# Kernel tuning notes

Measured on AMD Instinct MI355X. Metric: run time of the kernel, lower is better.

## Reference

```python
import jax, jax.numpy as jnp
import numpy as np


def setup_inputs() -> dict:
    key = jax.random.key(0)
    k1, k2 = jax.random.split(key)
    B, N, M, D = 16, 2048, 2048, 128
    Q = jax.random.normal(k1, (B, N, D), dtype=jnp.float32)
    KV = jax.random.normal(k2, (B, D, M), dtype=jnp.float32)
    log_sigmas = jnp.zeros((1,), dtype=jnp.float32)
    return {"Q": Q, "KV": KV, "log_sigmas": log_sigmas}


def reference(Q, KV, log_sigmas):
    # Q: [B, N, D], KV: [B, D, M]
    # ||q||^2 per row, ||k||^2 per column (norm squared == sum of squares)
    Q_sq = jnp.sum(Q * Q, axis=-1, keepdims=True)        # [B, N, 1]
    KV_sq = jnp.sum(KV * KV, axis=-2, keepdims=True)     # [B, 1, M]
    QKV = jnp.einsum('bnd,bdm->bnm', Q, KV)              # [B, N, M]
    inv_two_sigma_sq = -0.5 / jnp.exp(2.0 * log_sigmas)  # scalar (shape [1])
    # exp(-||q-k||^2 / (2 sigma^2)) fused epilogue
    out = jnp.exp(inv_two_sigma_sq * (Q_sq + KV_sq - 2.0 * QKV))
    return out
```

## Files before the change

kernel.cpp:

```cpp
#include <hip/hip_runtime.h>


#define B_  16
#define N_  2048
#define M_  2048
#define D_  128

typedef _Float16 half8 __attribute__((ext_vector_type(8)));
typedef float    f32x4 __attribute__((ext_vector_type(4)));

__global__ __launch_bounds__(256) void prep_q(const float* __restrict__ Q,
                                              _Float16* __restrict__ Qh,
                                              float* __restrict__ Qsq) {
    const int row  = blockIdx.x * 4 + (threadIdx.x >> 6);
    const int lane = threadIdx.x & 63;
    const float2 v = reinterpret_cast<const float2*>(Q + (size_t)row * D_)[lane];
    float sq = v.x * v.x + v.y * v.y;
    union { _Float16 h[2]; unsigned int u; } pk;
    pk.h[0] = (_Float16)v.x;
    pk.h[1] = (_Float16)v.y;
    reinterpret_cast<unsigned int*>(Qh + (size_t)row * D_)[lane] = pk.u;
    #pragma unroll
    for (int off = 32; off > 0; off >>= 1) sq += __shfl_down(sq, off, 64);
    if (lane == 0) Qsq[row] = sq;
}

__global__ __launch_bounds__(256) void prep_kv(const float* __restrict__ KV,
                                               _Float16* __restrict__ KTh,
                                               float* __restrict__ Ksq) {
    const int b = blockIdx.y;
    const int m = blockIdx.x * 256 + threadIdx.x;
    const float* src = KV + (size_t)b * D_ * M_ + m;
    _Float16*   dst = KTh + ((size_t)b * M_ + m) * D_;
    float sq = 0.f;
    #pragma unroll 2
    for (int k0 = 0; k0 < D_; k0 += 8) {
        union { _Float16 h[8]; int4 v; } buf;
        #pragma unroll
        for (int j = 0; j < 8; ++j) {
            const float v = src[(size_t)(k0 + j) * M_];
            sq += v * v;
            buf.h[j] = (_Float16)v;
        }
        *reinterpret_cast<int4*>(dst + k0) = buf.v;
    }
    Ksq[(size_t)b * M_ + m] = sq;
}

__global__ __launch_bounds__(256, 3) void gauss_gemm(
    const _Float16* __restrict__ Qh, const _Float16* __restrict__ KTh,
    const float* __restrict__ Qsq,  const float* __restrict__ Ksq,
    const float* __restrict__ ls,   float* __restrict__ out) {
    __shared__ __align__(16) _Float16 Ash[128 * 64];
    __shared__ __align__(16) _Float16 Bsh[128 * 64];

    const int b    = blockIdx.y;
    const int bx   = blockIdx.x;
    const int n0   = (bx >> 4) << 7;
    const int m0   = (bx & 15) << 7;
    const int tid  = threadIdx.x;
    const int wave = tid >> 6;
    const int lane = tid & 63;

    const _Float16* Ag = Qh  + ((size_t)b * N_ + n0) * D_;
    const _Float16* Bg = KTh + ((size_t)b * M_ + m0) * D_;

    int goff[4];
    #pragma unroll
    for (int j = 0; j < 4; ++j) {
        const int gi = j * 256 + tid;
        const int r  = gi >> 3;
        const int gc = gi & 7;
        goff[j] = r * D_ + ((gc ^ (r & 7)) << 3);
    }
    const int dbase = wave * 512;

    auto STAGE = [&](int h) {
        #pragma unroll
        for (int j = 0; j < 4; ++j) {
            __builtin_amdgcn_global_load_lds(
                (const __attribute__((address_space(1))) unsigned int*)(Ag + h * 64 + goff[j]),
                (__attribute__((address_space(3))) unsigned int*)(&Ash[j * 2048 + dbase]), 16, 0, 0);
            __builtin_amdgcn_global_load_lds(
                (const __attribute__((address_space(1))) unsigned int*)(Bg + h * 64 + goff[j]),
                (__attribute__((address_space(3))) unsigned int*)(&Bsh[j * 2048 + dbase]), 16, 0, 0);
        }
    };

    const int wr  = (wave >> 1) << 6;
    const int wc  = (wave & 1) << 6;
    const int lm  = lane & 15;
    const int kq  = lane >> 4;
    const int fsw = lm & 7;

    auto READ = [&](half8 af[2][4], half8 bf[2][4]) {
        #pragma unroll
        for (int s = 0; s < 2; ++s) {
            const int pc = ((((s << 2) + kq) ^ fsw) << 3);
            #pragma unroll
            for (int rr = 0; rr < 4; ++rr)
                af[s][rr] = *reinterpret_cast<const half8*>(
                    &Ash[(wr + rr * 16 + lm) * 64 + pc]);
            #pragma unroll
            for (int cc = 0; cc < 4; ++cc)
                bf[s][cc] = *reinterpret_cast<const half8*>(
                    &Bsh[(wc + cc * 16 + lm) * 64 + pc]);
        }
    };

    f32x4 acc[4][4] = {};
    auto MFMA = [&](half8 af[2][4], half8 bf[2][4]) {
        #pragma unroll
        for (int s = 0; s < 2; ++s)
            #pragma unroll
            for (int rr = 0; rr < 4; ++rr)
                #pragma unroll
                for (int cc = 0; cc < 4; ++cc)
                    acc[rr][cc] = __builtin_amdgcn_mfma_f32_16x16x32_f16(
                        af[s][rr], bf[s][cc], acc[rr][cc], 0, 0, 0);
    };

    STAGE(0);
    __syncthreads();

    half8 a0[2][4], b0[2][4];
    READ(a0, b0);
    __syncthreads();

    STAGE(1);
    MFMA(a0, b0);
    __syncthreads();

    half8 a1[2][4], b1[2][4];
    READ(a1, b1);
    MFMA(a1, b1);

    const float inv2s = -0.5f * __expf(-2.0f * ls[0]);
    const float cm2   = -2.0f * inv2s;
    const int   l4    = kq << 2;
    const float* qsq = Qsq + (size_t)b * N_ + n0;
    const float* ksq = Ksq + (size_t)b * M_ + m0;

    float ksv[4];
    #pragma unroll
    for (int cc = 0; cc < 4; ++cc) ksv[cc] = inv2s * ksq[wc + cc * 16 + lm];
    float qsv[4][4];
    #pragma unroll
    for (int rr = 0; rr < 4; ++rr)
        #pragma unroll
        for (int i = 0; i < 4; ++i) qsv[rr][i] = inv2s * qsq[wr + rr * 16 + l4 + i];

    float* Cb = out + ((size_t)b * N_ + n0 + wr + l4) * M_ + m0 + wc + lm;
    #pragma unroll
    for (int rr = 0; rr < 4; ++rr) {
        #pragma unroll
        for (int i = 0; i < 4; ++i) {
            float* p = Cb + (size_t)(rr * 16 + i) * M_;
            #pragma unroll
            for (int cc = 0; cc < 4; ++cc) {
                const float t = fmaf(cm2, acc[rr][cc][i], qsv[rr][i] + ksv[cc]);
                p[cc * 16] = __expf(t);
            }
        }
    }
}

extern "C" void kernel_launch(void* const* d_in, const int* in_sizes, int n_in,
                              void* d_out, int out_size, void* d_ws, size_t ws_size,
                              hipStream_t stream) {
    const float* Q  = (const float*)d_in[0];
    const float* KV = (const float*)d_in[1];
    const float* ls = (const float*)d_in[2];
    float* out = (float*)d_out;

    char* ws = (char*)d_ws;
    _Float16* Qh  = (_Float16*)ws;
    _Float16* KTh = (_Float16*)(ws + (size_t)8 * 1024 * 1024);
    float*    Qsq = (float*)(ws + (size_t)16 * 1024 * 1024);
    float*    Ksq = (float*)(ws + (size_t)16 * 1024 * 1024 + 128 * 1024);

    prep_q <<<dim3(B_ * N_ / 4), 256, 0, stream>>>(Q, Qh, Qsq);
    prep_kv<<<dim3(M_ / 256, B_), 256, 0, stream>>>(KV, KTh, Ksq);
    gauss_gemm<<<dim3(256, B_), 256, 0, stream>>>(Qh, KTh, Qsq, Ksq, ls, out);
}
```

Baseline: 307.8 us.

## Fuse prep kernels, swap MFMA operands for vectorized float4 output stores

Merges the Q and KV preprocessing into one launch and gives each KV column four waves that split the D dimension, with partial sums of squares combined through shared memory. Swaps the MFMA A/B operands so each lane's accumulator holds four consecutive output columns, which lets the epilogue write 16-byte vector stores instead of scalar strided stores. This targets launch overhead, low parallelism in the KV transpose, and store efficiency on the large fp32 output, at the cost of a transposed accumulator layout and a shared-memory reduction in the prep kernel.

```diff
diff --git a/kernel.cpp b/kernel.cpp
--- a/kernel.cpp
+++ b/kernel.cpp
@@ -9,42 +9,52 @@
 typedef _Float16 half8 __attribute__((ext_vector_type(8)));
 typedef float    f32x4 __attribute__((ext_vector_type(4)));
 
-__global__ __launch_bounds__(256) void prep_q(const float* __restrict__ Q,
-                                              _Float16* __restrict__ Qh,
-                                              float* __restrict__ Qsq) {
-    const int row  = blockIdx.x * 4 + (threadIdx.x >> 6);
-    const int lane = threadIdx.x & 63;
-    const float2 v = reinterpret_cast<const float2*>(Q + (size_t)row * D_)[lane];
-    float sq = v.x * v.x + v.y * v.y;
-    union { _Float16 h[2]; unsigned int u; } pk;
-    pk.h[0] = (_Float16)v.x;
-    pk.h[1] = (_Float16)v.y;
-    reinterpret_cast<unsigned int*>(Qh + (size_t)row * D_)[lane] = pk.u;
-    #pragma unroll
-    for (int off = 32; off > 0; off >>= 1) sq += __shfl_down(sq, off, 64);
-    if (lane == 0) Qsq[row] = sq;
-}
-
-__global__ __launch_bounds__(256) void prep_kv(const float* __restrict__ KV,
-                                               _Float16* __restrict__ KTh,
-                                               float* __restrict__ Ksq) {
-    const int b = blockIdx.y;
-    const int m = blockIdx.x * 256 + threadIdx.x;
-    const float* src = KV + (size_t)b * D_ * M_ + m;
-    _Float16*   dst = KTh + ((size_t)b * M_ + m) * D_;
-    float sq = 0.f;
-    #pragma unroll 2
-    for (int k0 = 0; k0 < D_; k0 += 8) {
-        union { _Float16 h[8]; int4 v; } buf;
+__global__ __launch_bounds__(256) void prep_all(const float* __restrict__ Q,
+                                                const float* __restrict__ KV,
+                                                _Float16* __restrict__ Qh,
+                                                float* __restrict__ Qsq,
+                                                _Float16* __restrict__ KTh,
+                                                float* __restrict__ Ksq) {
+    const int tid = threadIdx.x;
+    if (blockIdx.x < 512) {
+        __shared__ float part[4][64];
+        const int bx  = blockIdx.x;
+        const int b   = bx >> 5;
+        const int m0  = (bx & 31) << 6;
+        const int col = tid & 63;
+        const int wv  = tid >> 6;
+        const int m   = m0 + col;
+        const float* src = KV + (size_t)b * D_ * M_ + (size_t)(wv * 32) * M_ + m;
+        _Float16*    dst = KTh + ((size_t)b * M_ + m) * D_ + wv * 32;
+        float sq = 0.f;
+        union { _Float16 h[32]; int4 v[4]; } buf;
         #pragma unroll
-        for (int j = 0; j < 8; ++j) {
-            const float v = src[(size_t)(k0 + j) * M_];
-            sq += v * v;
+        for (int j = 0; j < 32; ++j) {
+            const float v = src[(size_t)j * M_];
+            sq = fmaf(v, v, sq);
             buf.h[j] = (_Float16)v;
         }
-        *reinterpret_cast<int4*>(dst + k0) = buf.v;
+        #pragma unroll
+        for (int j = 0; j < 4; ++j)
+            reinterpret_cast<int4*>(dst)[j] = buf.v[j];
+        part[wv][col] = sq;
+        __syncthreads();
+        if (wv == 0)
+            Ksq[(size_t)b * M_ + m] =
+                part[0][col] + part[1][col] + part[2][col] + part[3][col];
+    } else {
+        const int row  = (blockIdx.x - 512) * 4 + (tid >> 6);
+        const int lane = tid & 63;
+        const float2 v = reinterpret_cast<const float2*>(Q + (size_t)row * D_)[lane];
+        float sq = v.x * v.x + v.y * v.y;
+        union { _Float16 h[2]; unsigned int u; } pk;
+        pk.h[0] = (_Float16)v.x;
+        pk.h[1] = (_Float16)v.y;
+        reinterpret_cast<unsigned int*>(Qh + (size_t)row * D_)[lane] = pk.u;
+        #pragma unroll
+        for (int off = 32; off > 0; off >>= 1) sq += __shfl_down(sq, off, 64);
+        if (lane == 0) Qsq[row] = sq;
     }
-    Ksq[(size_t)b * M_ + m] = sq;
 }
 
 __global__ __launch_bounds__(256, 3) void gauss_gemm(
@@ -117,7 +127,7 @@
                 #pragma unroll
                 for (int cc = 0; cc < 4; ++cc)
                     acc[rr][cc] = __builtin_amdgcn_mfma_f32_16x16x32_f16(
-                        af[s][rr], bf[s][cc], acc[rr][cc], 0, 0, 0);
+                        bf[s][cc], af[s][rr], acc[rr][cc], 0, 0, 0);
     };
 
     STAGE(0);
@@ -137,30 +147,31 @@
 
     const float inv2s = -0.5f * __expf(-2.0f * ls[0]);
     const float cm2   = -2.0f * inv2s;
-    const int   l4    = kq << 2;
     const float* qsq = Qsq + (size_t)b * N_ + n0;
     const float* ksq = Ksq + (size_t)b * M_ + m0;
 
-    float ksv[4];
+    float qv[4];
     #pragma unroll
-    for (int cc = 0; cc < 4; ++cc) ksv[cc] = inv2s * ksq[wc + cc * 16 + lm];
-    float qsv[4][4];
+    for (int rr = 0; rr < 4; ++rr) qv[rr] = inv2s * qsq[wr + rr * 16 + lm];
+    f32x4 kv[4];
     #pragma unroll
-    for (int rr = 0; rr < 4; ++rr)
+    for (int cc = 0; cc < 4; ++cc) {
+        const f32x4 kr = *reinterpret_cast<const f32x4*>(&ksq[wc + cc * 16 + (kq << 2)]);
         #pragma unroll
-        for (int i = 0; i < 4; ++i) qsv[rr][i] = inv2s * qsq[wr + rr * 16 + l4 + i];
+        for (int e = 0; e < 4; ++e) kv[cc][e] = inv2s * kr[e];
+    }
 
-    float* Cb = out + ((size_t)b * N_ + n0 + wr + l4) * M_ + m0 + wc + lm;
+    float* Cb = out + ((size_t)b * N_ + n0 + wr + lm) * M_ + m0 + wc + (kq << 2);
     #pragma unroll
     for (int rr = 0; rr < 4; ++rr) {
+        float* p = Cb + (size_t)(rr * 16) * M_;
         #pragma unroll
-        for (int i = 0; i < 4; ++i) {
-            float* p = Cb + (size_t)(rr * 16 + i) * M_;
+        for (int cc = 0; cc < 4; ++cc) {
+            f32x4 v;
             #pragma unroll
-            for (int cc = 0; cc < 4; ++cc) {
-                const float t = fmaf(cm2, acc[rr][cc][i], qsv[rr][i] + ksv[cc]);
-                p[cc * 16] = __expf(t);
-            }
+            for (int e = 0; e < 4; ++e)
+                v[e] = __expf(fmaf(cm2, acc[rr][cc][e], qv[rr] + kv[cc][e]));
+            *reinterpret_cast<f32x4*>(p + cc * 16) = v;
         }
     }
 }
@@ -179,7 +190,6 @@
     float*    Qsq = (float*)(ws + (size_t)16 * 1024 * 1024);
     float*    Ksq = (float*)(ws + (size_t)16 * 1024 * 1024 + 128 * 1024);
 
-    prep_q <<<dim3(B_ * N_ / 4), 256, 0, stream>>>(Q, Qh, Qsq);
-    prep_kv<<<dim3(M_ / 256, B_), 256, 0, stream>>>(KV, KTh, Ksq);
+    prep_all<<<dim3(512 + B_ * N_ / 4), 256, 0, stream>>>(Q, KV, Qh, Qsq, KTh, Ksq);
     gauss_gemm<<<dim3(256, B_), 256, 0, stream>>>(Qh, KTh, Qsq, Ksq, ls, out);
 }
```

Result: no change. 305.6 us (-0.7%).
